# Kernel tuning notes

Hardware: AMD Instinct MI355X
Metric: run time of the kernel (lower is better)

The kernel has to match this reference:

```python
import jax, jax.numpy as jnp
import numpy as np

B, C, H, W = 4, 64, 64, 64
INTER = max(1, C // 8)


def setup_inputs() -> dict:
    key = jax.random.key(0)
    ks = jax.random.split(key, 8)
    return {
        "x": jax.random.normal(ks[0], (B, C, H, W), dtype=jnp.float32),
        "Wq": jax.random.normal(ks[1], (INTER, C), dtype=jnp.float32) * 0.1,
        "bq": jax.random.normal(ks[2], (INTER,), dtype=jnp.float32) * 0.1,
        "Wk": jax.random.normal(ks[3], (INTER, C), dtype=jnp.float32) * 0.1,
        "bk": jax.random.normal(ks[4], (INTER,), dtype=jnp.float32) * 0.1,
        "Wv": jax.random.normal(ks[5], (C, C), dtype=jnp.float32) * 0.1,
        "bv": jax.random.normal(ks[6], (C,), dtype=jnp.float32) * 0.1,
        "gamma": jax.random.normal(ks[7], (1,), dtype=jnp.float32),
    }


def reference(x, Wq, bq, Wk, bk, Wv, bv, gamma):
    b, c, h, w = x.shape
    n = h * w
    xf = x.reshape(b, c, n)  # flatten spatial dims, [B, C, N]
    # 1x1 convs == per-pixel matmuls
    q = jnp.einsum('ic,bcn->bin', Wq, xf) + bq[None, :, None]  # [B, inter, N]
    k = jnp.einsum('ic,bcn->bin', Wk, xf) + bk[None, :, None]  # [B, inter, N]
    v = jnp.einsum('oc,bcn->bon', Wv, xf) + bv[None, :, None]  # [B, C, N]
    # energy[b,n,m] = sum_i q[b,i,n] * k[b,i,m]  (unscaled attention)
    energy = jnp.einsum('bin,bim->bnm', q, k)  # [B, N, N]
    attn = jax.nn.softmax(energy, axis=-1)
    # out[b,c,n] = sum_m v[b,c,m] * attn[b,n,m]
    out = jnp.einsum('bcm,bnm->bcn', v, attn).reshape(b, c, h, w)
    return gamma[0] * out + x
```

## Files before the change

kernel.cpp:

```cpp
#include <hip/hip_runtime.h>


#define NPIX 4096
typedef __attribute__((ext_vector_type(8))) short s8v;
typedef __attribute__((ext_vector_type(4))) float f4v;

static __device__ __forceinline__ unsigned short f2bf(float f) {
    union { float f; unsigned u; } v; v.f = f;
    unsigned r = v.u + 0x7FFFu + ((v.u >> 16) & 1u);
    return (unsigned short)(r >> 16);
}

extern "C" __global__ void __launch_bounds__(256) qkv_kernel(
    const float* __restrict__ x,
    const float* __restrict__ Wq, const float* __restrict__ bq,
    const float* __restrict__ Wk, const float* __restrict__ bk,
    const float* __restrict__ Wv, const float* __restrict__ bv,
    unsigned short* __restrict__ qt, unsigned short* __restrict__ kt,
    unsigned short* __restrict__ vb)
{
    __shared__ float xls[64][65];
    __shared__ float wls[80][65];
    __shared__ float bls[80];
    const int t = threadIdx.x;
    const int b = blockIdx.x >> 6, n0 = (blockIdx.x & 63) << 6;

    for (int e = t; e < 4096; e += 256) {
        int c = e >> 6, j = e & 63;
        xls[c][j] = x[((b << 6) + c) * NPIX + n0 + j];
    }
    for (int e = t; e < 5120; e += 256) {
        int row = e >> 6, cc = e & 63;
        float wv = (e < 512) ? Wq[e] : (e < 1024) ? Wk[e - 512] : Wv[e - 1024];
        wls[row][cc] = wv;
    }
    if (t < 80) bls[t] = (t < 8) ? bq[t] : (t < 16) ? bk[t - 8] : bv[t - 16];
    __syncthreads();

    const int w = t >> 6, lane = t & 63, g = lane >> 4, c16 = lane & 15;

    s8v bfr[2];
#pragma unroll
    for (int s = 0; s < 2; ++s) {
        union { s8v v; unsigned short h[8]; } u;
#pragma unroll
        for (int j = 0; j < 8; ++j) u.h[j] = f2bf(xls[s * 32 + g * 8 + j][w * 16 + c16]);
        bfr[s] = u.v;
    }
    s8v afr[5][2];
#pragma unroll
    for (int rs = 0; rs < 5; ++rs)
#pragma unroll
        for (int s = 0; s < 2; ++s) {
            union { s8v v; unsigned short h[8]; } u;
#pragma unroll
            for (int j = 0; j < 8; ++j) u.h[j] = f2bf(wls[rs * 16 + c16][s * 32 + g * 8 + j]);
            afr[rs][s] = u.v;
        }

    f4v acc[5];
#pragma unroll
    for (int rs = 0; rs < 5; ++rs) { acc[rs][0]=0.f; acc[rs][1]=0.f; acc[rs][2]=0.f; acc[rs][3]=0.f; }
#pragma unroll
    for (int rs = 0; rs < 5; ++rs)
#pragma unroll
        for (int s = 0; s < 2; ++s)
            acc[rs] = __builtin_amdgcn_mfma_f32_16x16x32_bf16(afr[rs][s], bfr[s], acc[rs], 0, 0, 0);

    const int n = n0 + w * 16 + c16;
#pragma unroll
    for (int rs = 0; rs < 5; ++rs)
#pragma unroll
        for (int r = 0; r < 4; ++r) {
            int row = rs * 16 + g * 4 + r;
            unsigned short h = f2bf(acc[rs][r] + bls[row]);
            if (rs == 0) {
                if (row < 8) qt[(b * NPIX + n) * 8 + row] = h;
                else         kt[(b * NPIX + n) * 8 + row - 8] = h;
            } else {
                vb[((b << 6) + (row - 16)) * NPIX + n] = h;
            }
        }
}

extern "C" __global__ void __launch_bounds__(256) attn_kernel(
    const unsigned short* __restrict__ qt, const unsigned short* __restrict__ kt,
    const unsigned short* __restrict__ vb,
    const float* __restrict__ x, const float* __restrict__ gamma_p,
    float* __restrict__ out)
{
    __shared__ __align__(16) unsigned short vls[2][64][64];
    __shared__ __align__(16) unsigned short pls[4][16][72];
    __shared__ float lls[4][16];

    const int t = threadIdx.x;
    const int w = t >> 6, lane = t & 63, g = lane >> 4, c16 = lane & 15;
    const int b = blockIdx.x >> 6, n0 = (blockIdx.x & 63) << 6;

    const unsigned short* qtB = qt + b * NPIX * 8;
    const unsigned short* ktB = kt + b * NPIX * 8;
    const unsigned short* vbB = vb + (b << 6) * NPIX;

    s8v qfr = {0,0,0,0,0,0,0,0};
    if (g == 0) qfr = *(const s8v*)(qtB + (n0 + w * 16 + c16) * 8);

    const int vc = t >> 2, vq = t & 3;
    const int p0 = (2 * vq)     ^ (vc & 7);
    const int p1 = (2 * vq + 1) ^ (vc & 7);

    f4v accO[4];
#pragma unroll
    for (int cs = 0; cs < 4; ++cs) { accO[cs][0]=0.f; accO[cs][1]=0.f; accO[cs][2]=0.f; accO[cs][3]=0.f; }
    float lsum[4] = {0.f, 0.f, 0.f, 0.f};

    s8v vr0, vr1, kf[4], kfn[4];
    {
        const unsigned short* vp = vbB + vc * NPIX + vq * 16;
        vr0 = *(const s8v*)(vp);
        vr1 = *(const s8v*)(vp + 8);
#pragma unroll
        for (int ms = 0; ms < 4; ++ms) {
            s8v z = {0,0,0,0,0,0,0,0};
            kf[ms] = z;
            if (g == 0) kf[ms] = *(const s8v*)(ktB + (ms * 16 + c16) * 8);
        }
    }

    int cur = 0;
    for (int ti = 0; ti < 64; ++ti) {
        *(s8v*)&vls[cur][vc][p0 * 8] = vr0;
        *(s8v*)&vls[cur][vc][p1 * 8] = vr1;
        __syncthreads();

        if (ti < 63) {
            const int m1 = (ti + 1) << 6;
            const unsigned short* vp = vbB + vc * NPIX + m1 + vq * 16;
            vr0 = *(const s8v*)(vp);
            vr1 = *(const s8v*)(vp + 8);
#pragma unroll
            for (int ms = 0; ms < 4; ++ms) {
                s8v z = {0,0,0,0,0,0,0,0};
                kfn[ms] = z;
                if (g == 0) kfn[ms] = *(const s8v*)(ktB + (m1 + ms * 16 + c16) * 8);
            }
        }

        f4v sm[4];
#pragma unroll
        for (int ms = 0; ms < 4; ++ms) {
            f4v z; z[0]=0.f; z[1]=0.f; z[2]=0.f; z[3]=0.f;
            sm[ms] = __builtin_amdgcn_mfma_f32_16x16x32_bf16(qfr, kf[ms], z, 0, 0, 0);
        }

#pragma unroll
        for (int ms = 0; ms < 4; ++ms)
#pragma unroll
            for (int r = 0; r < 4; ++r) {
                float p = __expf(sm[ms][r]);
                lsum[r] += p;
                pls[w][g * 4 + r][ms * 16 + c16] = f2bf(p);
            }
        __builtin_amdgcn_wave_barrier();

        s8v pf0 = *(const s8v*)&pls[w][c16][g * 8];
        s8v pf1 = *(const s8v*)&pls[w][c16][32 + g * 8];

#pragma unroll
        for (int cs = 0; cs < 4; ++cs) {
            const int c = cs * 16 + c16;
            const int q0 = (g)     ^ (c16 & 7);
            const int q1 = (4 + g) ^ (c16 & 7);
            s8v vf0 = *(const s8v*)&vls[cur][c][q0 * 8];
            s8v vf1 = *(const s8v*)&vls[cur][c][q1 * 8];
            accO[cs] = __builtin_amdgcn_mfma_f32_16x16x32_bf16(vf0, pf0, accO[cs], 0, 0, 0);
            accO[cs] = __builtin_amdgcn_mfma_f32_16x16x32_bf16(vf1, pf1, accO[cs], 0, 0, 0);
        }

#pragma unroll
        for (int ms = 0; ms < 4; ++ms) kf[ms] = kfn[ms];
        cur ^= 1;
    }

#pragma unroll
    for (int r = 0; r < 4; ++r) {
        float L = lsum[r];
        L += __shfl_xor(L, 1); L += __shfl_xor(L, 2);
        L += __shfl_xor(L, 4); L += __shfl_xor(L, 8);
        lsum[r] = L;
    }
    if (c16 == 0) {
#pragma unroll
        for (int r = 0; r < 4; ++r) lls[w][g * 4 + r] = lsum[r];
    }
    __builtin_amdgcn_wave_barrier();
    const float ls = lls[w][c16];
    const float inv = 1.0f / ls;
    const float gm = gamma_p[0];

    const int n = n0 + w * 16 + c16;
#pragma unroll
    for (int cs = 0; cs < 4; ++cs)
#pragma unroll
        for (int r = 0; r < 4; ++r) {
            const int c = cs * 16 + g * 4 + r;
            const int gi = ((b << 6) + c) * NPIX + n;
            out[gi] = gm * (accO[cs][r] * inv) + x[gi];
        }
}

extern "C" void kernel_launch(void* const* d_in, const int* in_sizes, int n_in,
                              void* d_out, int out_size, void* d_ws, size_t ws_size,
                              hipStream_t stream) {
    const float* x     = (const float*)d_in[0];
    const float* Wq    = (const float*)d_in[1];
    const float* bq    = (const float*)d_in[2];
    const float* Wk    = (const float*)d_in[3];
    const float* bk    = (const float*)d_in[4];
    const float* Wv    = (const float*)d_in[5];
    const float* bv    = (const float*)d_in[6];
    const float* gamma = (const float*)d_in[7];

    unsigned short* qt = (unsigned short*)d_ws;
    unsigned short* kt = qt + 4 * NPIX * 8;
    unsigned short* vb = kt + 4 * NPIX * 8;

    qkv_kernel<<<256, 256, 0, stream>>>(x, Wq, bq, Wk, bk, Wv, bv, qt, kt, vb);
    attn_kernel<<<256, 256, 0, stream>>>(qt, kt, vb, x, gamma, (float*)d_out);
}
```

Baseline: 129.8 us.

## Split attention over key dimension with partial sums and combine kernel

The attention kernel now splits the key range into S slices, launching S times more blocks, and writes partial output and row-sum buffers that a new combine kernel reduces and normalises. The point is to fill more of the GPU's compute units than 256 blocks can. The QKV projection is rewritten as a scalar FP32 FMA kernel over 16-pixel tiles with 1024 blocks instead of MFMA. V double buffering is replaced by a single LDS buffer with an extra barrier per tile. The split path costs extra global traffic for the partials and one more launch, and it depends on workspace size.

```diff
diff --git a/kernel.cpp b/kernel.cpp
--- a/kernel.cpp
+++ b/kernel.cpp
@@ -19,83 +19,67 @@
     unsigned short* __restrict__ qt, unsigned short* __restrict__ kt,
     unsigned short* __restrict__ vb)
 {
-    __shared__ float xls[64][65];
-    __shared__ float wls[80][65];
+    __shared__ float xs[64][17];
+    __shared__ __align__(16) float wls[80][68];
     __shared__ float bls[80];
     const int t = threadIdx.x;
-    const int b = blockIdx.x >> 6, n0 = (blockIdx.x & 63) << 6;
-
-    for (int e = t; e < 4096; e += 256) {
-        int c = e >> 6, j = e & 63;
-        xls[c][j] = x[((b << 6) + c) * NPIX + n0 + j];
+    const int b = blockIdx.x >> 8, n0 = (blockIdx.x & 255) << 4;
+
+    for (int e = t; e < 1024; e += 256) {
+        int c = e >> 4, j = e & 15;
+        xs[c][j] = x[((b << 6) + c) * NPIX + n0 + j];
     }
     for (int e = t; e < 5120; e += 256) {
         int row = e >> 6, cc = e & 63;
-        float wv = (e < 512) ? Wq[e] : (e < 1024) ? Wk[e - 512] : Wv[e - 1024];
-        wls[row][cc] = wv;
+        wls[row][cc] = (e < 512) ? Wq[e] : (e < 1024) ? Wk[e - 512] : Wv[e - 1024];
     }
     if (t < 80) bls[t] = (t < 8) ? bq[t] : (t < 16) ? bk[t - 8] : bv[t - 16];
     __syncthreads();
 
-    const int w = t >> 6, lane = t & 63, g = lane >> 4, c16 = lane & 15;
-
-    s8v bfr[2];
-#pragma unroll
-    for (int s = 0; s < 2; ++s) {
-        union { s8v v; unsigned short h[8]; } u;
-#pragma unroll
-        for (int j = 0; j < 8; ++j) u.h[j] = f2bf(xls[s * 32 + g * 8 + j][w * 16 + c16]);
-        bfr[s] = u.v;
-    }
-    s8v afr[5][2];
-#pragma unroll
-    for (int rs = 0; rs < 5; ++rs)
-#pragma unroll
-        for (int s = 0; s < 2; ++s) {
-            union { s8v v; unsigned short h[8]; } u;
-#pragma unroll
-            for (int j = 0; j < 8; ++j) u.h[j] = f2bf(wls[rs * 16 + c16][s * 32 + g * 8 + j]);
-            afr[rs][s] = u.v;
-        }
-
-    f4v acc[5];
-#pragma unroll
-    for (int rs = 0; rs < 5; ++rs) { acc[rs][0]=0.f; acc[rs][1]=0.f; acc[rs][2]=0.f; acc[rs][3]=0.f; }
-#pragma unroll
-    for (int rs = 0; rs < 5; ++rs)
-#pragma unroll
-        for (int s = 0; s < 2; ++s)
-            acc[rs] = __builtin_amdgcn_mfma_f32_16x16x32_bf16(afr[rs][s], bfr[s], acc[rs], 0, 0, 0);
-
-    const int n = n0 + w * 16 + c16;
-#pragma unroll
-    for (int rs = 0; rs < 5; ++rs)
-#pragma unroll
-        for (int r = 0; r < 4; ++r) {
-            int row = rs * 16 + g * 4 + r;
-            unsigned short h = f2bf(acc[rs][r] + bls[row]);
-            if (rs == 0) {
-                if (row < 8) qt[(b * NPIX + n) * 8 + row] = h;
-                else         kt[(b * NPIX + n) * 8 + row - 8] = h;
-            } else {
-                vb[((b << 6) + (row - 16)) * NPIX + n] = h;
-            }
-        }
-}
-
-extern "C" __global__ void __launch_bounds__(256) attn_kernel(
+    const int j = t & 15, oh = t >> 4;
+    float xr[64];
+#pragma unroll
+    for (int c = 0; c < 64; ++c) xr[c] = xs[c][j];
+
+    const int n = n0 + j;
+#pragma unroll
+    for (int r = 0; r < 5; ++r) {
+        const int row = oh * 5 + r;
+        float acc = bls[row];
+#pragma unroll
+        for (int q = 0; q < 16; ++q) {
+            float4 wv = *(const float4*)&wls[row][q * 4];
+            acc += wv.x * xr[4*q] + wv.y * xr[4*q+1] + wv.z * xr[4*q+2] + wv.w * xr[4*q+3];
+        }
+        const unsigned short h = f2bf(acc);
+        if (row < 8)       qt[(b * NPIX + n) * 8 + row] = h;
+        else if (row < 16) kt[(b * NPIX + n) * 8 + row - 8] = h;
+        else               vb[((b << 6) + (row - 16)) * NPIX + n] = h;
+    }
+}
+
+template<int S, bool DIRECT>
+__global__ __launch_bounds__(256) void attn_kern(
     const unsigned short* __restrict__ qt, const unsigned short* __restrict__ kt,
     const unsigned short* __restrict__ vb,
     const float* __restrict__ x, const float* __restrict__ gamma_p,
-    float* __restrict__ out)
+    float* __restrict__ out, float* __restrict__ Opart, float* __restrict__ Lpart)
 {
-    __shared__ __align__(16) unsigned short vls[2][64][64];
+    constexpr int LS = (S == 1) ? 0 : (S == 2) ? 1 : 2;
+    constexpr int TC = 64 / S;
+
+    __shared__ __align__(16) unsigned short vls[64][64];
     __shared__ __align__(16) unsigned short pls[4][16][72];
     __shared__ float lls[4][16];
 
     const int t = threadIdx.x;
     const int w = t >> 6, lane = t & 63, g = lane >> 4, c16 = lane & 15;
-    const int b = blockIdx.x >> 6, n0 = (blockIdx.x & 63) << 6;
+    const int bid = blockIdx.x;
+    const int s  = bid & (S - 1);
+    const int nt = (bid >> LS) & 63;
+    const int b  = bid >> (LS + 6);
+    const int n0 = nt << 6;
+    const int tb = s * TC;
 
     const unsigned short* qtB = qt + b * NPIX * 8;
     const unsigned short* ktB = kt + b * NPIX * 8;
@@ -115,25 +99,25 @@
 
     s8v vr0, vr1, kf[4], kfn[4];
     {
-        const unsigned short* vp = vbB + vc * NPIX + vq * 16;
+        const int m0 = tb << 6;
+        const unsigned short* vp = vbB + vc * NPIX + m0 + vq * 16;
         vr0 = *(const s8v*)(vp);
         vr1 = *(const s8v*)(vp + 8);
 #pragma unroll
         for (int ms = 0; ms < 4; ++ms) {
             s8v z = {0,0,0,0,0,0,0,0};
             kf[ms] = z;
-            if (g == 0) kf[ms] = *(const s8v*)(ktB + (ms * 16 + c16) * 8);
-        }
-    }
-
-    int cur = 0;
-    for (int ti = 0; ti < 64; ++ti) {
-        *(s8v*)&vls[cur][vc][p0 * 8] = vr0;
-        *(s8v*)&vls[cur][vc][p1 * 8] = vr1;
+            if (g == 0) kf[ms] = *(const s8v*)(ktB + (m0 + ms * 16 + c16) * 8);
+        }
+    }
+
+    for (int ti = 0; ti < TC; ++ti) {
+        *(s8v*)&vls[vc][p0 * 8] = vr0;
+        *(s8v*)&vls[vc][p1 * 8] = vr1;
         __syncthreads();
 
-        if (ti < 63) {
-            const int m1 = (ti + 1) << 6;
+        if (ti < TC - 1) {
+            const int m1 = (tb + ti + 1) << 6;
             const unsigned short* vp = vbB + vc * NPIX + m1 + vq * 16;
             vr0 = *(const s8v*)(vp);
             vr1 = *(const s8v*)(vp + 8);
@@ -170,15 +154,15 @@
             const int c = cs * 16 + c16;
             const int q0 = (g)     ^ (c16 & 7);
             const int q1 = (4 + g) ^ (c16 & 7);
-            s8v vf0 = *(const s8v*)&vls[cur][c][q0 * 8];
-            s8v vf1 = *(const s8v*)&vls[cur][c][q1 * 8];
+            s8v vf0 = *(const s8v*)&vls[c][q0 * 8];
+            s8v vf1 = *(const s8v*)&vls[c][q1 * 8];
             accO[cs] = __builtin_amdgcn_mfma_f32_16x16x32_bf16(vf0, pf0, accO[cs], 0, 0, 0);
             accO[cs] = __builtin_amdgcn_mfma_f32_16x16x32_bf16(vf1, pf1, accO[cs], 0, 0, 0);
         }
+        __syncthreads();
 
 #pragma unroll
         for (int ms = 0; ms < 4; ++ms) kf[ms] = kfn[ms];
-        cur ^= 1;
     }
 
 #pragma unroll
@@ -188,24 +172,66 @@
         L += __shfl_xor(L, 4); L += __shfl_xor(L, 8);
         lsum[r] = L;
     }
-    if (c16 == 0) {
-#pragma unroll
-        for (int r = 0; r < 4; ++r) lls[w][g * 4 + r] = lsum[r];
-    }
-    __builtin_amdgcn_wave_barrier();
-    const float ls = lls[w][c16];
-    const float inv = 1.0f / ls;
+
+    const int n = n0 + w * 16 + c16;
+    if constexpr (DIRECT) {
+        if (c16 == 0) {
+#pragma unroll
+            for (int r = 0; r < 4; ++r) lls[w][g * 4 + r] = lsum[r];
+        }
+        __builtin_amdgcn_wave_barrier();
+        const float inv = 1.0f / lls[w][c16];
+        const float gm = gamma_p[0];
+#pragma unroll
+        for (int cs = 0; cs < 4; ++cs)
+#pragma unroll
+            for (int r = 0; r < 4; ++r) {
+                const int c = cs * 16 + g * 4 + r;
+                const int gi = ((b << 6) + c) * NPIX + n;
+                out[gi] = gm * (accO[cs][r] * inv) + x[gi];
+            }
+    } else {
+        (void)lls;
+#pragma unroll
+        for (int cs = 0; cs < 4; ++cs)
+#pragma unroll
+            for (int r = 0; r < 4; ++r) {
+                const int c = cs * 16 + g * 4 + r;
+                Opart[((((s << 2) + b) << 6) + c) * NPIX + n] = accO[cs][r];
+            }
+        if (c16 == 0) {
+#pragma unroll
+            for (int r = 0; r < 4; ++r)
+                Lpart[(((s << 2) + b) * NPIX) + n0 + w * 16 + g * 4 + r] = lsum[r];
+        }
+    }
+}
+
+template<int S>
+__global__ __launch_bounds__(256) void combine_kern(
+    const float* __restrict__ Opart, const float* __restrict__ Lpart,
+    const float* __restrict__ x, const float* __restrict__ gamma_p,
+    float* __restrict__ out)
+{
+    const int tid = blockIdx.x * 256 + threadIdx.x;
+    const int e = tid << 2;
+    const int n = e & 4095, c = (e >> 12) & 63, b = e >> 18;
+    float4 o = {0.f,0.f,0.f,0.f}, l = {0.f,0.f,0.f,0.f};
+#pragma unroll
+    for (int s = 0; s < S; ++s) {
+        float4 ov = *(const float4*)&Opart[((((s << 2) + b) << 6) + c) * NPIX + n];
+        float4 lv = *(const float4*)&Lpart[(((s << 2) + b) * NPIX) + n];
+        o.x += ov.x; o.y += ov.y; o.z += ov.z; o.w += ov.w;
+        l.x += lv.x; l.y += lv.y; l.z += lv.z; l.w += lv.w;
+    }
     const float gm = gamma_p[0];
-
-    const int n = n0 + w * 16 + c16;
-#pragma unroll
-    for (int cs = 0; cs < 4; ++cs)
-#pragma unroll
-        for (int r = 0; r < 4; ++r) {
-            const int c = cs * 16 + g * 4 + r;
-            const int gi = ((b << 6) + c) * NPIX + n;
-            out[gi] = gm * (accO[cs][r] * inv) + x[gi];
-        }
+    float4 xv = *(const float4*)&x[e];
+    float4 r;
+    r.x = gm * o.x / l.x + xv.x;
+    r.y = gm * o.y / l.y + xv.y;
+    r.z = gm * o.z / l.z + xv.z;
+    r.w = gm * o.w / l.w + xv.w;
+    *(float4*)&out[e] = r;
 }
 
 extern "C" void kernel_launch(void* const* d_in, const int* in_sizes, int n_in,
@@ -223,7 +249,22 @@
     unsigned short* qt = (unsigned short*)d_ws;
     unsigned short* kt = qt + 4 * NPIX * 8;
     unsigned short* vb = kt + 4 * NPIX * 8;
-
-    qkv_kernel<<<256, 256, 0, stream>>>(x, Wq, bq, Wk, bk, Wv, bv, qt, kt, vb);
-    attn_kernel<<<256, 256, 0, stream>>>(qt, kt, vb, x, gamma, (float*)d_out);
-}
+    float* Opart = (float*)(vb + 4 * 64 * NPIX);
+    const size_t base = (size_t)(4 * NPIX * 8) * 2 * 2 + (size_t)4 * 64 * NPIX * 2;
+    const size_t per_slice = (size_t)4 * 64 * NPIX * 4 + (size_t)4 * NPIX * 4;
+
+    float* out = (float*)d_out;
+    qkv_kernel<<<1024, 256, 0, stream>>>(x, Wq, bq, Wk, bk, Wv, bv, qt, kt, vb);
+
+    if (ws_size >= base + 4 * per_slice) {
+        float* Lpart = Opart + (size_t)4 * 4 * 64 * NPIX;
+        attn_kern<4, false><<<1024, 256, 0, stream>>>(qt, kt, vb, x, gamma, out, Opart, Lpart);
+        combine_kern<4><<<1024, 256, 0, stream>>>(Opart, Lpart, x, gamma, out);
+    } else if (ws_size >= base + 2 * per_slice) {
+        float* Lpart = Opart + (size_t)2 * 4 * 64 * NPIX;
+        attn_kern<2, false><<<512, 256, 0, stream>>>(qt, kt, vb, x, gamma, out, Opart, Lpart);
+        combine_kern<2><<<1024, 256, 0, stream>>>(Opart, Lpart, x, gamma, out);
+    } else {
+        attn_kern<1, true><<<256, 256, 0, stream>>>(qt, kt, vb, x, gamma, out, nullptr, nullptr);
+    }
+}
```

Measured after the change: 114.7 us. 1.13x faster.
